# Kernel optimization log

Hardware: AMD Instinct MI355X
Metric: run time of the kernel (lower is better)

## Reference

```python
import jax, jax.numpy as jnp
import numpy as np

SEQ, BATCH, IN = 512, 256, 15
H1, H2, FC_HID, NUM_CLASSES = 512, 512, 64, 1


def setup_inputs() -> dict:
    key = jax.random.key(0)
    ks = jax.random.split(key, 14)
    def u(k, shape, fan_in):
        b = 1.0 / np.sqrt(fan_in)
        return jax.random.uniform(k, shape, jnp.float32, -b, b)
    return {
        "x": jax.random.normal(ks[0], (SEQ, BATCH, IN), jnp.float32),
        # PyTorch LSTM params, gate order i,f,g,o stacked along dim 0
        "W_ih1": u(ks[1], (4 * H1, IN), H1),
        "W_hh1": u(ks[2], (4 * H1, H1), H1),
        "b_ih1": u(ks[3], (4 * H1,), H1),
        "b_hh1": u(ks[4], (4 * H1,), H1),
        "W_ih2": u(ks[5], (4 * H2, H1), H2),
        "W_hh2": u(ks[6], (4 * H2, H2), H2),
        "b_ih2": u(ks[7], (4 * H2,), H2),
        "b_hh2": u(ks[8], (4 * H2,), H2),
        "fc1_w": u(ks[9], (FC_HID, H2), H2),
        "fc1_b": u(ks[10], (FC_HID,), H2),
        "fc_w": u(ks[11], (NUM_CLASSES, FC_HID), FC_HID),
        "fc_b": u(ks[12], (NUM_CLASSES,), FC_HID),
    }


def _lstm_cell(x_t, h, c, W_ih, W_hh, b_ih, b_hh):
    # gates: [B, 4H], PyTorch gate order i, f, g, o
    g = x_t @ W_ih.T + b_ih + h @ W_hh.T + b_hh
    i, f, gg, o = jnp.split(g, 4, axis=-1)
    c_new = jax.nn.sigmoid(f) * c + jax.nn.sigmoid(i) * jnp.tanh(gg)
    h_new = jax.nn.sigmoid(o) * jnp.tanh(c_new)
    return h_new, c_new


def reference(x, W_ih1, W_hh1, b_ih1, b_hh1, W_ih2, W_hh2, b_ih2, b_hh2,
              fc1_w, fc1_b, fc_w, fc_b):
    S, B, _ = x.shape
    init = (jnp.zeros((B, H1), x.dtype), jnp.zeros((B, H1), x.dtype),
            jnp.zeros((B, H2), x.dtype), jnp.zeros((B, H2), x.dtype))

    def step(carry, x_t):
        h1, c1, h2, c2 = carry
        h1, c1 = _lstm_cell(x_t, h1, c1, W_ih1, W_hh1, b_ih1, b_hh1)
        h2, c2 = _lstm_cell(h1, h2, c2, W_ih2, W_hh2, b_ih2, b_hh2)
        return (h1, c1, h2, c2), None

    (h1, c1, h2, c2), _ = jax.lax.scan(step, init, x)
    # MLP head on final-timestep top-layer hidden state; `out += out` doubles it
    hn = jax.nn.relu(h2)
    out = jax.nn.relu(hn @ fc1_w.T + fc1_b)
    out = out @ fc_w.T + fc_b
    return out + out
```

## Files before the change

### kernel.cpp

```cpp
#include <hip/hip_runtime.h>
#include <cstdint>
#include <cstddef>

typedef __attribute__((ext_vector_type(8))) short short8;
typedef __attribute__((ext_vector_type(4))) float floatx4;

constexpr int kSeq = 512;
constexpr int kBatch = 256;
constexpr int kIn = 15;
constexpr int kH = 512;
constexpr int kG = 4 * kH;
constexpr int kRing = 17;
constexpr size_t kHSlot = (size_t)kBatch * kH;
constexpr size_t kShmemBytes = 131072 + 4096;

__device__ __forceinline__ unsigned short f2bf(float f) {
    union { float f; unsigned u; } v; v.f = f;
    unsigned u = v.u;
    return (unsigned short)((u + 0x7fffu + ((u >> 16) & 1u)) >> 16);
}

__device__ __forceinline__ float sigm(float x) { return 1.0f / (1.0f + __expf(-x)); }
__device__ __forceinline__ float tanh_(float x) { return 1.0f - 2.0f / (1.0f + __expf(2.0f * x)); }

#define LLC_STORE16(P, V)                                                     \
    asm volatile("global_store_dwordx4 %0, %1, off sc0 sc1"                   \
                 :: "v"(P), "v"(V) : "memory")

__device__ __forceinline__ void waitf(const int* flags, int tgt, int lane, int& fc) {
    if (tgt <= 0) return;
    bool watch = (lane < 32);
    if (__all(!watch || fc >= tgt)) return;
    int spin = 0;
    for (;;) {
        if (watch && fc < tgt)
            fc = __hip_atomic_load(flags + lane * 16,
                                   __ATOMIC_RELAXED, __HIP_MEMORY_SCOPE_AGENT);
        if (__all(!watch || fc >= tgt)) return;
        if (++spin > 4096) __builtin_amdgcn_s_sleep(8);
    }
}

__global__ void k_conv(const float* __restrict__ src, unsigned short* __restrict__ dst, int n) {
    int i = blockIdx.x * blockDim.x + threadIdx.x;
    if (i < n) dst[i] = f2bf(src[i]);
}

__global__ void k_conv_pad(const float* __restrict__ src, unsigned short* __restrict__ dst, int rows) {
    int i = blockIdx.x * blockDim.x + threadIdx.x;
    if (i >= rows * 32) return;
    int r = i >> 5, k = i & 31;
    dst[i] = (k < kIn) ? f2bf(src[r * kIn + k]) : (unsigned short)0;
}

__global__ __launch_bounds__(256) void k_persist(
    const unsigned short* __restrict__ whh1b,
    const unsigned short* __restrict__ wih1b,
    const unsigned short* __restrict__ wih2b,
    const unsigned short* __restrict__ whh2b,
    const unsigned short* __restrict__ xb,
    const float* __restrict__ bih1, const float* __restrict__ bhh1,
    const float* __restrict__ bih2, const float* __restrict__ bhh2,
    unsigned short* __restrict__ h1r,
    unsigned short* __restrict__ h2r,
    float* __restrict__ h2f,
    int* __restrict__ flags)
{
    extern __shared__ unsigned short lw[];
    const int bid = blockIdx.x;
    const int g = bid & 3;
    const int role = bid >> 2;
    const bool is2 = role >= 32;
    const int rid = role & 31;
    const int j0 = rid << 4;
    const int tid = (int)threadIdx.x;
    const int wave = tid >> 6;
    const int lane = tid & 63;
    const int lcol = lane & 15;
    const int quad = lane >> 4;
    const int m0 = (g << 6) + wave * 16;
    const int arow = m0 + lcol;
    const int koff = quad * 8;

    int* f1 = flags + g * 1024;
    int* f2 = f1 + 512;
    int* myflag = (is2 ? f2 : f1) + rid * 16;
    unsigned short* scr = lw + 65536 + wave * 384;

    if (!is2) {
        for (int i = tid; i < 4096; i += 256) {
            int ln = i >> 6, gg = ln >> 4, u = ln & 15;
            int c = i & 63, kk = c >> 2, qd = c & 3;
            *(short8*)&lw[((gg * 16 + kk) << 9) + ((qd * 16 + u) << 3)] =
                *(const short8*)&whh1b[(size_t)((gg << 9) + j0 + u) * kH + c * 8];
        }
        for (int i = tid; i < 256; i += 256) {
            int ln = i >> 2, gg = ln >> 4, u = ln & 15;
            int qd = i & 3;
            *(short8*)&lw[((64 + gg) << 9) + ((qd * 16 + u) << 3)] =
                *(const short8*)&wih1b[((gg << 9) + j0 + u) * 32 + qd * 8];
        }
    } else {
        for (int i = tid; i < 4096; i += 256) {
            int ln = i >> 6, gg = ln >> 4, u = ln & 15;
            int c = i & 63, kk = c >> 2, qd = c & 3;
            int dst = ((gg * 16 + kk) << 9) + ((qd * 16 + u) << 3);
            size_t src = (size_t)((gg << 9) + j0 + u) * kH + c * 8;
            *(short8*)&lw[dst] = *(const short8*)&wih2b[src];
            *(short8*)&lw[dst + (64 << 9)] = *(const short8*)&whh2b[src];
        }
    }
    float bsum[4];
#pragma unroll
    for (int gg = 0; gg < 4; ++gg) {
        int n = (gg << 9) + j0 + lcol;
        bsum[gg] = is2 ? (bih2[n] + bhh2[n]) : (bih1[n] + bhh1[n]);
    }
    __syncthreads();

    float creg[4] = {0.f, 0.f, 0.f, 0.f};
    int fc1 = 0, fc2 = 0;

    if (!is2) {
        for (int s = 0; s < kSeq; ++s) {
            if ((s & 15) == 0) {
                waitf(f1, s, lane, fc1);
                waitf(f2, s, lane, fc2);
                __builtin_amdgcn_fence(__ATOMIC_ACQUIRE, "agent");
            }
            floatx4 acc[4];
#pragma unroll
            for (int gg = 0; gg < 4; ++gg)
                acc[gg] = (floatx4){bsum[gg], bsum[gg], bsum[gg], bsum[gg]};

            short8 ax = *(const short8*)(xb + ((size_t)s * kBatch + arow) * 32 + koff);

            waitf(f1, s, lane, fc1);
            const unsigned short* hp = h1r + (size_t)((s + 16) % kRing) * kHSlot
                                       + (size_t)arow * kH + koff;
            short8 a[16];
#pragma unroll
            for (int kk = 0; kk < 16; ++kk) a[kk] = *(const short8*)(hp + kk * 32);
#pragma unroll
            for (int kk = 0; kk < 16; ++kk) {
#pragma unroll
                for (int gg = 0; gg < 4; ++gg) {
                    short8 b = *(const short8*)&lw[((gg * 16 + kk) << 9) + (lane << 3)];
                    acc[gg] = __builtin_amdgcn_mfma_f32_16x16x32_bf16(a[kk], b, acc[gg], 0, 0, 0);
                }
            }
#pragma unroll
            for (int gg = 0; gg < 4; ++gg) {
                short8 b = *(const short8*)&lw[((64 + gg) << 9) + (lane << 3)];
                acc[gg] = __builtin_amdgcn_mfma_f32_16x16x32_bf16(ax, b, acc[gg], 0, 0, 0);
            }

            unsigned short* hw = h1r + (size_t)(s % kRing) * kHSlot;
#pragma unroll
            for (int r = 0; r < 4; ++r) {
                int row = quad * 4 + r;
                float gi = acc[0][r], gf = acc[1][r], ggv = acc[2][r], go = acc[3][r];
                float cn = sigm(gf) * creg[r] + sigm(gi) * tanh_(ggv);
                float hn = sigm(go) * tanh_(cn);
                creg[r] = cn;
                scr[row * 24 + lcol] = f2bf(hn);
            }
            if (lane < 32) {
                int row = lane >> 1, seg = lane & 1;
                short8 v = *(short8*)&scr[row * 24 + seg * 8];
                unsigned short* gp = hw + (size_t)(m0 + row) * kH + j0 + seg * 8;
                LLC_STORE16(gp, v);
            }
            __builtin_amdgcn_s_waitcnt(0);
            __syncthreads();
            if (tid == 0)
                __hip_atomic_store(myflag, s + 1,
                                   __ATOMIC_RELAXED, __HIP_MEMORY_SCOPE_AGENT);
        }
    } else {
        for (int u = 0; u < kSeq; ++u) {
            if ((u & 15) == 0) {
                waitf(f1, u, lane, fc1);
                waitf(f2, u, lane, fc2);
                __builtin_amdgcn_fence(__ATOMIC_ACQUIRE, "agent");
            }
            floatx4 acc[4];
#pragma unroll
            for (int gg = 0; gg < 4; ++gg)
                acc[gg] = (floatx4){bsum[gg], bsum[gg], bsum[gg], bsum[gg]};

            waitf(f2, u, lane, fc2);

            const unsigned short* hp2 = h2r + (size_t)((u + 16) % kRing) * kHSlot
                                        + (size_t)arow * kH + koff;
            short8 a[16];
#pragma unroll
            for (int kk = 0; kk < 16; ++kk) a[kk] = *(const short8*)(hp2 + kk * 32);
#pragma unroll
            for (int kk = 0; kk < 16; ++kk) {
#pragma unroll
                for (int gg = 0; gg < 4; ++gg) {
                    short8 b = *(const short8*)&lw[((64 + gg * 16 + kk) << 9) + (lane << 3)];
                    acc[gg] = __builtin_amdgcn_mfma_f32_16x16x32_bf16(a[kk], b, acc[gg], 0, 0, 0);
                }
            }

            waitf(f1, u + 1, lane, fc1);

            const unsigned short* hp1 = h1r + (size_t)(u % kRing) * kHSlot
                                        + (size_t)arow * kH + koff;
#pragma unroll
            for (int kk = 0; kk < 16; ++kk) a[kk] = *(const short8*)(hp1 + kk * 32);
#pragma unroll
            for (int kk = 0; kk < 16; ++kk) {
#pragma unroll
                for (int gg = 0; gg < 4; ++gg) {
                    short8 b = *(const short8*)&lw[((gg * 16 + kk) << 9) + (lane << 3)];
                    acc[gg] = __builtin_amdgcn_mfma_f32_16x16x32_bf16(a[kk], b, acc[gg], 0, 0, 0);
                }
            }

            unsigned short* hw = h2r + (size_t)(u % kRing) * kHSlot;
            const int j = j0 + lcol;
#pragma unroll
            for (int r = 0; r < 4; ++r) {
                int row = quad * 4 + r;
                float gi = acc[0][r], gf = acc[1][r], ggv = acc[2][r], go = acc[3][r];
                float cn = sigm(gf) * creg[r] + sigm(gi) * tanh_(ggv);
                float hn = sigm(go) * tanh_(cn);
                creg[r] = cn;
                scr[row * 24 + lcol] = f2bf(hn);
                if (u == kSeq - 1) h2f[(size_t)(m0 + row) * kH + j] = hn;
            }
            if (lane < 32) {
                int row = lane >> 1, seg = lane & 1;
                short8 v = *(short8*)&scr[row * 24 + seg * 8];
                unsigned short* gp = hw + (size_t)(m0 + row) * kH + j0 + seg * 8;
                LLC_STORE16(gp, v);
            }
            __builtin_amdgcn_s_waitcnt(0);
            __syncthreads();
            if (tid == 0)
                __hip_atomic_store(myflag, u + 1,
                                   __ATOMIC_RELAXED, __HIP_MEMORY_SCOPE_AGENT);
        }
    }
}

__global__ __launch_bounds__(64) void k_head(
    const float* __restrict__ h2f, const float* __restrict__ fc1w,
    const float* __restrict__ fc1b, const float* __restrict__ fcw,
    const float* __restrict__ fcb, float* __restrict__ out)
{
    int m = blockIdx.x;
    int j = threadIdx.x;
    const float* hr = h2f + (size_t)m * kH;
    const float* wr = fc1w + (size_t)j * kH;
    float sacc = 0.f;
    for (int k = 0; k < kH; ++k) sacc += fmaxf(hr[k], 0.f) * wr[k];
    float rv = fmaxf(sacc + fc1b[j], 0.f) * fcw[j];
#pragma unroll
    for (int off = 32; off >= 1; off >>= 1) rv += __shfl_down(rv, off);
    if (j == 0) out[m] = 2.0f * (rv + fcb[0]);
}

extern "C" void kernel_launch(void* const* d_in, const int* in_sizes, int n_in,
                              void* d_out, int out_size, void* d_ws, size_t ws_size,
                              hipStream_t stream) {
    const float* x    = (const float*)d_in[0];
    const float* Wih1 = (const float*)d_in[1];
    const float* Whh1 = (const float*)d_in[2];
    const float* bih1 = (const float*)d_in[3];
    const float* bhh1 = (const float*)d_in[4];
    const float* Wih2 = (const float*)d_in[5];
    const float* Whh2 = (const float*)d_in[6];
    const float* bih2 = (const float*)d_in[7];
    const float* bhh2 = (const float*)d_in[8];
    const float* fc1w = (const float*)d_in[9];
    const float* fc1b = (const float*)d_in[10];
    const float* fcw  = (const float*)d_in[11];
    const float* fcb  = (const float*)d_in[12];
    float* out = (float*)d_out;

    char* p = (char*)d_ws;
    auto take = [&](size_t bytes) -> char* {
        char* r = p;
        p += (bytes + 255) & ~(size_t)255;
        return r;
    };
    unsigned short* whh1b = (unsigned short*)take((size_t)kG * kH * 2);
    unsigned short* wih2b = (unsigned short*)take((size_t)kG * kH * 2);
    unsigned short* whh2b = (unsigned short*)take((size_t)kG * kH * 2);
    unsigned short* wih1b = (unsigned short*)take((size_t)kG * 32 * 2);
    unsigned short* xb    = (unsigned short*)take((size_t)kSeq * kBatch * 32 * 2);
    char* state = p;
    unsigned short* h1r = (unsigned short*)take((size_t)kRing * kHSlot * 2);
    unsigned short* h2r = (unsigned short*)take((size_t)kRing * kHSlot * 2);
    int* flags = (int*)take(16384);
    size_t state_bytes = (size_t)((char*)flags + 16384 - state);
    float* h2f = (float*)take((size_t)kBatch * kH * 4);

    hipMemsetAsync(state, 0, state_bytes, stream);

    int n = kG * kH;
    k_conv<<<(n + 255) / 256, 256, 0, stream>>>(Whh1, whh1b, n);
    k_conv<<<(n + 255) / 256, 256, 0, stream>>>(Wih2, wih2b, n);
    k_conv<<<(n + 255) / 256, 256, 0, stream>>>(Whh2, whh2b, n);
    k_conv_pad<<<(kG * 32 + 255) / 256, 256, 0, stream>>>(Wih1, wih1b, kG);
    k_conv_pad<<<(kSeq * kBatch * 32 + 255) / 256, 256, 0, stream>>>(x, xb, kSeq * kBatch);

    hipFuncSetAttribute((const void*)k_persist,
                        hipFuncAttributeMaxDynamicSharedMemorySize, (int)kShmemBytes);
    void* args[] = {&whh1b, &wih1b, &wih2b, &whh2b, &xb,
                    (void*)&bih1, (void*)&bhh1, (void*)&bih2, (void*)&bhh2,
                    &h1r, &h2r, &h2f, &flags};
    hipError_t e = hipLaunchCooperativeKernel((const void*)k_persist, dim3(256), dim3(256),
                                              args, (unsigned)kShmemBytes, stream);
    if (e != hipSuccess) {
        k_persist<<<256, 256, kShmemBytes, stream>>>(
            whh1b, wih1b, wih2b, whh2b, xb, bih1, bhh1, bih2, bhh2,
            h1r, h2r, h2f, flags);
    }

    k_head<<<kBatch, 64, 0, stream>>>(h2f, fc1w, fc1b, fcw, fcb, out);
}
```

Before: 4.164 ms.

## Replace per-step flag barriers with sentinel-poisoned ring slots and data polling

Drops the per-timestep waitcnt, syncthreads and flag store in both LSTM layers. Consumers instead load the hidden-state slot directly and re-poll any chunk still holding the 0xFFFF sentinel. Every 16 steps a two-phase boundary barrier re-poisons the next ring slots so stale data is detectable. The layer-1 input MFMA is moved to overlap the h load. This removes per-step synchronization latency but relies on the sentinel never equalling a real bf16 value (0xFFFF is a NaN pattern) and on store visibility ordering within 16-byte chunks.

```diff
diff --git a/kernel.cpp b/kernel.cpp
--- a/kernel.cpp
+++ b/kernel.cpp
@@ -39,6 +39,65 @@
         if (__all(!watch || fc >= tgt)) return;
         if (++spin > 4096) __builtin_amdgcn_s_sleep(8);
     }
+}
+
+__device__ __forceinline__ void issue16(short8* a, const unsigned short* hp, unsigned mask) {
+#pragma unroll
+    for (int kk = 0; kk < 16; ++kk)
+        if (mask & (1u << kk))
+            asm volatile("global_load_dwordx4 %0, %1, off sc0 sc1"
+                         : "=v"(a[kk]) : "v"(hp + (size_t)kk * 32) : "memory");
+}
+
+__device__ __forceinline__ void chunk_wait() {
+    asm volatile("s_waitcnt vmcnt(0)" ::: "memory");
+    __builtin_amdgcn_sched_barrier(0);
+}
+
+__device__ __forceinline__ unsigned stale_of(const short8* a, unsigned mask) {
+    unsigned st = 0;
+#pragma unroll
+    for (int kk = 0; kk < 16; ++kk)
+        if (mask & (1u << kk))
+            if (a[kk][0] == (short)-1 || a[kk][7] == (short)-1) st |= (1u << kk);
+    return st;
+}
+
+__device__ __forceinline__ void repoll(short8* a, const unsigned short* hp, unsigned stale) {
+    int spin = 0;
+    while (__any(stale != 0)) {
+        issue16(a, hp, stale);
+        chunk_wait();
+        stale = stale_of(a, stale);
+        if (++spin > 2048) __builtin_amdgcn_s_sleep(8);
+    }
+}
+
+__device__ __forceinline__ void boundary(
+    int B, unsigned short* ring, int g, int j0, int tid, int lane,
+    int* wfs, int* pfs, int* my_wf, int* my_pf,
+    int& cw1, int& cw2, int& cp1, int& cp2)
+{
+    __syncthreads();
+    if (tid == 0) __hip_atomic_store(my_wf, B, __ATOMIC_RELAXED, __HIP_MEMORY_SCOPE_AGENT);
+    waitf(wfs, B, lane, cw1);
+    waitf(wfs + 512, B, lane, cw2);
+    short8 pv;
+#pragma unroll
+    for (int j = 0; j < 8; ++j) pv[j] = (short)-1;
+#pragma unroll
+    for (int i = 0; i < 8; ++i) {
+        int c = tid * 8 + i;
+        int t = c >> 7, r = (c >> 1) & 63, seg = c & 1;
+        unsigned short* p = ring + (size_t)((B + t) % kRing) * kHSlot
+                            + (size_t)((g << 6) + r) * kH + j0 + seg * 8;
+        LLC_STORE16(p, pv);
+    }
+    __builtin_amdgcn_s_waitcnt(0);
+    __syncthreads();
+    if (tid == 0) __hip_atomic_store(my_pf, B, __ATOMIC_RELAXED, __HIP_MEMORY_SCOPE_AGENT);
+    waitf(pfs, B, lane, cp1);
+    waitf(pfs + 512, B, lane, cp2);
 }
 
 __global__ void k_conv(const float* __restrict__ src, unsigned short* __restrict__ dst, int n) {
@@ -82,9 +141,9 @@
     const int arow = m0 + lcol;
     const int koff = quad * 8;
 
-    int* f1 = flags + g * 1024;
-    int* f2 = f1 + 512;
-    int* myflag = (is2 ? f2 : f1) + rid * 16;
+    int* fg = flags + g * 2048;
+    int* my_wf = fg + (is2 ? 512 : 0) + rid * 16;
+    int* my_pf = my_wf + 1024;
     unsigned short* scr = lw + 65536 + wave * 384;
 
     if (!is2) {
@@ -119,28 +178,32 @@
     __syncthreads();
 
     float creg[4] = {0.f, 0.f, 0.f, 0.f};
-    int fc1 = 0, fc2 = 0;
+    int cw1 = 0, cw2 = 0, cp1 = 0, cp2 = 0;
 
     if (!is2) {
         for (int s = 0; s < kSeq; ++s) {
-            if ((s & 15) == 0) {
-                waitf(f1, s, lane, fc1);
-                waitf(f2, s, lane, fc2);
-                __builtin_amdgcn_fence(__ATOMIC_ACQUIRE, "agent");
-            }
+            if (s && !(s & 15))
+                boundary(s, h1r, g, j0, tid, lane, fg, fg + 1024, my_wf, my_pf,
+                         cw1, cw2, cp1, cp2);
             floatx4 acc[4];
 #pragma unroll
             for (int gg = 0; gg < 4; ++gg)
                 acc[gg] = (floatx4){bsum[gg], bsum[gg], bsum[gg], bsum[gg]};
 
-            short8 ax = *(const short8*)(xb + ((size_t)s * kBatch + arow) * 32 + koff);
-
-            waitf(f1, s, lane, fc1);
             const unsigned short* hp = h1r + (size_t)((s + 16) % kRing) * kHSlot
                                        + (size_t)arow * kH + koff;
             short8 a[16];
-#pragma unroll
-            for (int kk = 0; kk < 16; ++kk) a[kk] = *(const short8*)(hp + kk * 32);
+            issue16(a, hp, 0xFFFFu);
+
+            short8 ax = *(const short8*)(xb + ((size_t)s * kBatch + arow) * 32 + koff);
+#pragma unroll
+            for (int gg = 0; gg < 4; ++gg) {
+                short8 b = *(const short8*)&lw[((64 + gg) << 9) + (lane << 3)];
+                acc[gg] = __builtin_amdgcn_mfma_f32_16x16x32_bf16(ax, b, acc[gg], 0, 0, 0);
+            }
+            chunk_wait();
+            if (s > 0) repoll(a, hp, stale_of(a, 0xFFFFu));
+
 #pragma unroll
             for (int kk = 0; kk < 16; ++kk) {
 #pragma unroll
@@ -148,11 +211,6 @@
                     short8 b = *(const short8*)&lw[((gg * 16 + kk) << 9) + (lane << 3)];
                     acc[gg] = __builtin_amdgcn_mfma_f32_16x16x32_bf16(a[kk], b, acc[gg], 0, 0, 0);
                 }
-            }
-#pragma unroll
-            for (int gg = 0; gg < 4; ++gg) {
-                short8 b = *(const short8*)&lw[((64 + gg) << 9) + (lane << 3)];
-                acc[gg] = __builtin_amdgcn_mfma_f32_16x16x32_bf16(ax, b, acc[gg], 0, 0, 0);
             }
 
             unsigned short* hw = h1r + (size_t)(s % kRing) * kHSlot;
@@ -171,52 +229,46 @@
                 unsigned short* gp = hw + (size_t)(m0 + row) * kH + j0 + seg * 8;
                 LLC_STORE16(gp, v);
             }
-            __builtin_amdgcn_s_waitcnt(0);
-            __syncthreads();
-            if (tid == 0)
-                __hip_atomic_store(myflag, s + 1,
-                                   __ATOMIC_RELAXED, __HIP_MEMORY_SCOPE_AGENT);
         }
     } else {
         for (int u = 0; u < kSeq; ++u) {
-            if ((u & 15) == 0) {
-                waitf(f1, u, lane, fc1);
-                waitf(f2, u, lane, fc2);
-                __builtin_amdgcn_fence(__ATOMIC_ACQUIRE, "agent");
-            }
+            if (u && !(u & 15))
+                boundary(u, h2r, g, j0, tid, lane, fg, fg + 1024, my_wf, my_pf,
+                         cw1, cw2, cp1, cp2);
             floatx4 acc[4];
 #pragma unroll
             for (int gg = 0; gg < 4; ++gg)
                 acc[gg] = (floatx4){bsum[gg], bsum[gg], bsum[gg], bsum[gg]};
 
-            waitf(f2, u, lane, fc2);
-
             const unsigned short* hp2 = h2r + (size_t)((u + 16) % kRing) * kHSlot
                                         + (size_t)arow * kH + koff;
-            short8 a[16];
-#pragma unroll
-            for (int kk = 0; kk < 16; ++kk) a[kk] = *(const short8*)(hp2 + kk * 32);
+            short8 a2[16];
+            issue16(a2, hp2, 0xFFFFu);
+            chunk_wait();
+            if (u > 0) repoll(a2, hp2, stale_of(a2, 0xFFFFu));
+
+            const unsigned short* hp1 = h1r + (size_t)(u % kRing) * kHSlot
+                                        + (size_t)arow * kH + koff;
+            short8 a1[16];
+            issue16(a1, hp1, 0xFFFFu);
+
 #pragma unroll
             for (int kk = 0; kk < 16; ++kk) {
 #pragma unroll
                 for (int gg = 0; gg < 4; ++gg) {
                     short8 b = *(const short8*)&lw[((64 + gg * 16 + kk) << 9) + (lane << 3)];
-                    acc[gg] = __builtin_amdgcn_mfma_f32_16x16x32_bf16(a[kk], b, acc[gg], 0, 0, 0);
+                    acc[gg] = __builtin_amdgcn_mfma_f32_16x16x32_bf16(a2[kk], b, acc[gg], 0, 0, 0);
                 }
             }
-
-            waitf(f1, u + 1, lane, fc1);
-
-            const unsigned short* hp1 = h1r + (size_t)(u % kRing) * kHSlot
-                                        + (size_t)arow * kH + koff;
-#pragma unroll
-            for (int kk = 0; kk < 16; ++kk) a[kk] = *(const short8*)(hp1 + kk * 32);
+            chunk_wait();
+            repoll(a1, hp1, stale_of(a1, 0xFFFFu));
+
 #pragma unroll
             for (int kk = 0; kk < 16; ++kk) {
 #pragma unroll
                 for (int gg = 0; gg < 4; ++gg) {
                     short8 b = *(const short8*)&lw[((gg * 16 + kk) << 9) + (lane << 3)];
-                    acc[gg] = __builtin_amdgcn_mfma_f32_16x16x32_bf16(a[kk], b, acc[gg], 0, 0, 0);
+                    acc[gg] = __builtin_amdgcn_mfma_f32_16x16x32_bf16(a1[kk], b, acc[gg], 0, 0, 0);
                 }
             }
 
@@ -238,11 +290,6 @@
                 unsigned short* gp = hw + (size_t)(m0 + row) * kH + j0 + seg * 8;
                 LLC_STORE16(gp, v);
             }
-            __builtin_amdgcn_s_waitcnt(0);
-            __syncthreads();
-            if (tid == 0)
-                __hip_atomic_store(myflag, u + 1,
-                                   __ATOMIC_RELAXED, __HIP_MEMORY_SCOPE_AGENT);
         }
     }
 }
@@ -293,14 +340,16 @@
     unsigned short* whh2b = (unsigned short*)take((size_t)kG * kH * 2);
     unsigned short* wih1b = (unsigned short*)take((size_t)kG * 32 * 2);
     unsigned short* xb    = (unsigned short*)take((size_t)kSeq * kBatch * 32 * 2);
-    char* state = p;
     unsigned short* h1r = (unsigned short*)take((size_t)kRing * kHSlot * 2);
     unsigned short* h2r = (unsigned short*)take((size_t)kRing * kHSlot * 2);
-    int* flags = (int*)take(16384);
-    size_t state_bytes = (size_t)((char*)flags + 16384 - state);
+    int* flags = (int*)take(32768);
     float* h2f = (float*)take((size_t)kBatch * kH * 4);
 
-    hipMemsetAsync(state, 0, state_bytes, stream);
+    hipMemsetAsync(h1r, 0xFF, (size_t)kRing * kHSlot * 2, stream);
+    hipMemsetAsync(h2r, 0xFF, (size_t)kRing * kHSlot * 2, stream);
+    hipMemsetAsync(h1r + (size_t)16 * kHSlot, 0, kHSlot * 2, stream);
+    hipMemsetAsync(h2r + (size_t)16 * kHSlot, 0, kHSlot * 2, stream);
+    hipMemsetAsync(flags, 0, 32768, stream);
 
     int n = kG * kH;
     k_conv<<<(n + 255) / 256, 256, 0, stream>>>(Whh1, whh1b, n);
```

Result: slower. 6.276 ms (+50.7%).

## Use per-wave progress flags and add an idle spinning wave

Applied to the files above, without the earlier changes.

Each wave now publishes and waits on its own progress flag instead of the whole block meeting at a barrier every timestep. Waves working on different batch rows can therefore advance independently, which removes block-wide barrier stalls from the recurrence. A fifth wave is added that runs dummy FMA loops until the four compute waves signal completion through shared memory, apparently to keep the compute unit busy or its clocks high. The extra wave costs power and issue slots and makes the launch wider, and the per-wave flags depend on each wave only reading rows that the matching waves of other blocks produce.

```diff
diff --git a/kernel.cpp b/kernel.cpp
--- a/kernel.cpp
+++ b/kernel.cpp
@@ -53,7 +53,7 @@
     dst[i] = (k < kIn) ? f2bf(src[r * kIn + k]) : (unsigned short)0;
 }
 
-__global__ __launch_bounds__(256) void k_persist(
+__global__ __launch_bounds__(320) void k_persist(
     const unsigned short* __restrict__ whh1b,
     const unsigned short* __restrict__ wih1b,
     const unsigned short* __restrict__ wih2b,
@@ -84,8 +84,30 @@
 
     int* f1 = flags + g * 1024;
     int* f2 = f1 + 512;
-    int* myflag = (is2 ? f2 : f1) + rid * 16;
+    int* dn = (int*)(lw + 67072);
+
+    if (wave == 4) {
+        __syncthreads();
+        float a0 = 1.0f, a1 = 1.25f, a2 = 1.5f, a3 = 1.75f;
+        float m = 1.0f, c = 1e-7f;
+        while (__hip_atomic_load(dn, __ATOMIC_RELAXED, __HIP_MEMORY_SCOPE_WORKGROUP) < 4) {
+            asm volatile(
+                ".rept 16\n\t"
+                "v_fmac_f32 %0, %4, %5\n\t"
+                "v_fmac_f32 %1, %4, %5\n\t"
+                "v_fmac_f32 %2, %4, %5\n\t"
+                "v_fmac_f32 %3, %4, %5\n\t"
+                ".endr"
+                : "+v"(a0), "+v"(a1), "+v"(a2), "+v"(a3)
+                : "v"(m), "v"(c));
+        }
+        return;
+    }
+
+    int* myflag = (is2 ? f2 : f1) + rid * 16 + wave;
     unsigned short* scr = lw + 65536 + wave * 384;
+
+    if (tid == 0) *dn = 0;
 
     if (!is2) {
         for (int i = tid; i < 4096; i += 256) {
@@ -124,8 +146,8 @@
     if (!is2) {
         for (int s = 0; s < kSeq; ++s) {
             if ((s & 15) == 0) {
-                waitf(f1, s, lane, fc1);
-                waitf(f2, s, lane, fc2);
+                waitf(f1 + wave, s, lane, fc1);
+                waitf(f2 + wave, s, lane, fc2);
                 __builtin_amdgcn_fence(__ATOMIC_ACQUIRE, "agent");
             }
             floatx4 acc[4];
@@ -135,7 +157,7 @@
 
             short8 ax = *(const short8*)(xb + ((size_t)s * kBatch + arow) * 32 + koff);
 
-            waitf(f1, s, lane, fc1);
+            waitf(f1 + wave, s, lane, fc1);
             const unsigned short* hp = h1r + (size_t)((s + 16) % kRing) * kHSlot
                                        + (size_t)arow * kH + koff;
             short8 a[16];
@@ -172,16 +194,15 @@
                 LLC_STORE16(gp, v);
             }
             __builtin_amdgcn_s_waitcnt(0);
-            __syncthreads();
-            if (tid == 0)
+            if (lane == 0)
                 __hip_atomic_store(myflag, s + 1,
                                    __ATOMIC_RELAXED, __HIP_MEMORY_SCOPE_AGENT);
         }
     } else {
         for (int u = 0; u < kSeq; ++u) {
             if ((u & 15) == 0) {
-                waitf(f1, u, lane, fc1);
-                waitf(f2, u, lane, fc2);
+                waitf(f1 + wave, u, lane, fc1);
+                waitf(f2 + wave, u, lane, fc2);
                 __builtin_amdgcn_fence(__ATOMIC_ACQUIRE, "agent");
             }
             floatx4 acc[4];
@@ -189,7 +210,7 @@
             for (int gg = 0; gg < 4; ++gg)
                 acc[gg] = (floatx4){bsum[gg], bsum[gg], bsum[gg], bsum[gg]};
 
-            waitf(f2, u, lane, fc2);
+            waitf(f2 + wave, u, lane, fc2);
 
             const unsigned short* hp2 = h2r + (size_t)((u + 16) % kRing) * kHSlot
                                         + (size_t)arow * kH + koff;
@@ -205,7 +226,7 @@
                 }
             }
 
-            waitf(f1, u + 1, lane, fc1);
+            waitf(f1 + wave, u + 1, lane, fc1);
 
             const unsigned short* hp1 = h1r + (size_t)(u % kRing) * kHSlot
                                         + (size_t)arow * kH + koff;
@@ -239,12 +260,14 @@
                 LLC_STORE16(gp, v);
             }
             __builtin_amdgcn_s_waitcnt(0);
-            __syncthreads();
-            if (tid == 0)
+            if (lane == 0)
                 __hip_atomic_store(myflag, u + 1,
                                    __ATOMIC_RELAXED, __HIP_MEMORY_SCOPE_AGENT);
         }
     }
+
+    if (lane == 0)
+        __hip_atomic_fetch_add(dn, 1, __ATOMIC_RELAXED, __HIP_MEMORY_SCOPE_WORKGROUP);
 }
 
 __global__ __launch_bounds__(64) void k_head(
@@ -314,10 +337,10 @@
     void* args[] = {&whh1b, &wih1b, &wih2b, &whh2b, &xb,
                     (void*)&bih1, (void*)&bhh1, (void*)&bih2, (void*)&bhh2,
                     &h1r, &h2r, &h2f, &flags};
-    hipError_t e = hipLaunchCooperativeKernel((const void*)k_persist, dim3(256), dim3(256),
+    hipError_t e = hipLaunchCooperativeKernel((const void*)k_persist, dim3(256), dim3(320),
                                               args, (unsigned)kShmemBytes, stream);
     if (e != hipSuccess) {
-        k_persist<<<256, 256, kShmemBytes, stream>>>(
+        k_persist<<<256, 320, kShmemBytes, stream>>>(
             whh1b, wih1b, wih2b, whh2b, xb, bih1, bhh1, bih2, bhh2,
             h1r, h2r, h2f, flags);
     }
```

Result: slower. 5.306 ms (+27.4%).

## Consume recurrent GEMM K-chunks as soon as each producer's flag is ready

Applied to the files above, without the earlier changes.

The recurrent h·W GEMMs no longer wait for all 32 producer flags before starting. A new consume_gemm helper polls the flags, builds a ballot mask of producer pairs that are ready, and issues the loads and MFMAs for each matching K-chunk as it becomes available. This overlaps the matrix work with the wait on slower producer blocks in the cross-block pipeline. The cost is extra ballot and bitmask logic, branchy code that may hurt unrolling, register allocation and instruction scheduling, and a different MFMA accumulation order.

```diff
diff --git a/kernel.cpp b/kernel.cpp
--- a/kernel.cpp
+++ b/kernel.cpp
@@ -29,15 +29,64 @@
 
 __device__ __forceinline__ void waitf(const int* flags, int tgt, int lane, int& fc) {
     if (tgt <= 0) return;
-    bool watch = (lane < 32);
-    if (__all(!watch || fc >= tgt)) return;
+    const int* myf = flags + (lane & 31) * 16;
     int spin = 0;
-    for (;;) {
-        if (watch && fc < tgt)
-            fc = __hip_atomic_load(flags + lane * 16,
-                                   __ATOMIC_RELAXED, __HIP_MEMORY_SCOPE_AGENT);
-        if (__all(!watch || fc >= tgt)) return;
+    while (!__all(fc >= tgt)) {
+        if (fc < tgt)
+            fc = __hip_atomic_load(myf, __ATOMIC_RELAXED, __HIP_MEMORY_SCOPE_AGENT);
         if (++spin > 4096) __builtin_amdgcn_s_sleep(8);
+    }
+}
+
+__device__ __forceinline__ void consume_gemm(
+    const int* flags, int tgt, int lane, int& fc,
+    const unsigned short* hp, const unsigned short* lw, int wbase,
+    floatx4* acc)
+{
+    short8 a[16];
+    if (tgt <= 0) {
+#pragma unroll
+        for (int kk = 0; kk < 16; ++kk) a[kk] = *(const short8*)(hp + kk * 32);
+#pragma unroll
+        for (int kk = 0; kk < 16; ++kk)
+#pragma unroll
+            for (int gg = 0; gg < 4; ++gg) {
+                short8 b = *(const short8*)&lw[((wbase + gg * 16 + kk) << 9) + (lane << 3)];
+                acc[gg] = __builtin_amdgcn_mfma_f32_16x16x32_bf16(a[kk], b, acc[gg], 0, 0, 0);
+            }
+        return;
+    }
+    const int* myf = flags + (lane & 31) * 16;
+    unsigned issued = 0;
+    int spin = 0;
+    while (issued != 0xFFFFu) {
+        if (fc < tgt)
+            fc = __hip_atomic_load(myf, __ATOMIC_RELAXED, __HIP_MEMORY_SCOPE_AGENT);
+        unsigned b32 = (unsigned)__ballot(fc >= tgt);
+        unsigned pairs = b32 & (b32 >> 1) & 0x55555555u;
+        unsigned newm = 0;
+#pragma unroll
+        for (int kk = 0; kk < 16; ++kk)
+            if ((pairs >> (2 * kk)) & 1u) newm |= 1u << kk;
+        newm &= ~issued;
+        if (newm) {
+#pragma unroll
+            for (int kk = 0; kk < 16; ++kk)
+                if ((newm >> kk) & 1u) a[kk] = *(const short8*)(hp + kk * 32);
+#pragma unroll
+            for (int kk = 0; kk < 16; ++kk)
+                if ((newm >> kk) & 1u) {
+#pragma unroll
+                    for (int gg = 0; gg < 4; ++gg) {
+                        short8 b = *(const short8*)&lw[((wbase + gg * 16 + kk) << 9) + (lane << 3)];
+                        acc[gg] = __builtin_amdgcn_mfma_f32_16x16x32_bf16(a[kk], b, acc[gg], 0, 0, 0);
+                    }
+                }
+            issued |= newm;
+            spin = 0;
+        } else if (++spin > 4096) {
+            __builtin_amdgcn_s_sleep(8);
+        }
     }
 }
 
@@ -134,26 +183,15 @@
                 acc[gg] = (floatx4){bsum[gg], bsum[gg], bsum[gg], bsum[gg]};
 
             short8 ax = *(const short8*)(xb + ((size_t)s * kBatch + arow) * 32 + koff);
-
-            waitf(f1, s, lane, fc1);
-            const unsigned short* hp = h1r + (size_t)((s + 16) % kRing) * kHSlot
-                                       + (size_t)arow * kH + koff;
-            short8 a[16];
-#pragma unroll
-            for (int kk = 0; kk < 16; ++kk) a[kk] = *(const short8*)(hp + kk * 32);
-#pragma unroll
-            for (int kk = 0; kk < 16; ++kk) {
-#pragma unroll
-                for (int gg = 0; gg < 4; ++gg) {
-                    short8 b = *(const short8*)&lw[((gg * 16 + kk) << 9) + (lane << 3)];
-                    acc[gg] = __builtin_amdgcn_mfma_f32_16x16x32_bf16(a[kk], b, acc[gg], 0, 0, 0);
-                }
-            }
 #pragma unroll
             for (int gg = 0; gg < 4; ++gg) {
                 short8 b = *(const short8*)&lw[((64 + gg) << 9) + (lane << 3)];
                 acc[gg] = __builtin_amdgcn_mfma_f32_16x16x32_bf16(ax, b, acc[gg], 0, 0, 0);
             }
+
+            const unsigned short* hp = h1r + (size_t)((s + 16) % kRing) * kHSlot
+                                       + (size_t)arow * kH + koff;
+            consume_gemm(f1, s, lane, fc1, hp, lw, 0, acc);
 
             unsigned short* hw = h1r + (size_t)(s % kRing) * kHSlot;
 #pragma unroll
@@ -189,36 +227,13 @@
             for (int gg = 0; gg < 4; ++gg)
                 acc[gg] = (floatx4){bsum[gg], bsum[gg], bsum[gg], bsum[gg]};
 
-            waitf(f2, u, lane, fc2);
-
             const unsigned short* hp2 = h2r + (size_t)((u + 16) % kRing) * kHSlot
                                         + (size_t)arow * kH + koff;
-            short8 a[16];
-#pragma unroll
-            for (int kk = 0; kk < 16; ++kk) a[kk] = *(const short8*)(hp2 + kk * 32);
-#pragma unroll
-            for (int kk = 0; kk < 16; ++kk) {
-#pragma unroll
-                for (int gg = 0; gg < 4; ++gg) {
-                    short8 b = *(const short8*)&lw[((64 + gg * 16 + kk) << 9) + (lane << 3)];
-                    acc[gg] = __builtin_amdgcn_mfma_f32_16x16x32_bf16(a[kk], b, acc[gg], 0, 0, 0);
-                }
-            }
-
-            waitf(f1, u + 1, lane, fc1);
+            consume_gemm(f2, u, lane, fc2, hp2, lw, 64, acc);
 
             const unsigned short* hp1 = h1r + (size_t)(u % kRing) * kHSlot
                                         + (size_t)arow * kH + koff;
-#pragma unroll
-            for (int kk = 0; kk < 16; ++kk) a[kk] = *(const short8*)(hp1 + kk * 32);
-#pragma unroll
-            for (int kk = 0; kk < 16; ++kk) {
-#pragma unroll
-                for (int gg = 0; gg < 4; ++gg) {
-                    short8 b = *(const short8*)&lw[((gg * 16 + kk) << 9) + (lane << 3)];
-                    acc[gg] = __builtin_amdgcn_mfma_f32_16x16x32_bf16(a[kk], b, acc[gg], 0, 0, 0);
-                }
-            }
+            consume_gemm(f1, u + 1, lane, fc1, hp1, lw, 0, acc);
 
             unsigned short* hw = h2r + (size_t)(u % kRing) * kHSlot;
             const int j = j0 + lcol;
```

After: 5.375 ms. 29.1% more time.
